# Kernel tuning notes

Measured on AMD Instinct MI355X. Metric: run time of the kernel, lower is better.

Reference implementation:

```python
import jax, jax.numpy as jnp
import numpy as np

NEG_SLOPE = 0.2

def _glorot(key, shape):
    fan_in, fan_out = shape[0], shape[1]
    lim = (6.0 / (fan_in + fan_out)) ** 0.5
    return jax.random.uniform(key, shape, jnp.float32, -lim, lim)

def setup_inputs() -> dict:
    key = jax.random.key(0)
    N, E = 50000, 1000000
    node_dim, edge_dim, hidden = 64, 16, 32
    H1 = 4
    ks = jax.random.split(key, 20)
    x = jax.random.normal(ks[0], (N, node_dim), jnp.float32)
    edge_index = jax.random.randint(ks[1], (2, E), 0, N, jnp.int64)
    edge_attr = jax.random.normal(ks[2], (E, edge_dim), jnp.float32)
    d = dict(x=x, edge_index=edge_index, edge_attr=edge_attr)
    # gat1: GATv2Conv(node_dim -> hidden, heads=4, edge_dim)
    d['W1l'] = _glorot(ks[3], (node_dim, H1 * hidden)); d['b1l'] = jnp.zeros((H1 * hidden,), jnp.float32)
    d['W1r'] = _glorot(ks[4], (node_dim, H1 * hidden)); d['b1r'] = jnp.zeros((H1 * hidden,), jnp.float32)
    d['W1e'] = _glorot(ks[5], (edge_dim, H1 * hidden))
    d['att1'] = _glorot(ks[6], (H1, hidden))
    d['bias1'] = jnp.zeros((H1 * hidden,), jnp.float32)
    # gat2: GATv2Conv(4*hidden -> hidden, heads=1, edge_dim)
    d['W2l'] = _glorot(ks[7], (H1 * hidden, hidden)); d['b2l'] = jnp.zeros((hidden,), jnp.float32)
    d['W2r'] = _glorot(ks[8], (H1 * hidden, hidden)); d['b2r'] = jnp.zeros((hidden,), jnp.float32)
    d['W2e'] = _glorot(ks[9], (edge_dim, hidden))
    d['att2'] = _glorot(ks[10], (1, hidden))
    d['bias2'] = jnp.zeros((hidden,), jnp.float32)
    # edge classifier: Linear(2*hidden+edge_dim -> hidden), ReLU, Linear(hidden -> 1)
    ein = 2 * hidden + edge_dim
    d['Wc1'] = _glorot(ks[11], (ein, hidden)); d['bc1'] = jnp.zeros((hidden,), jnp.float32)
    d['Wc2'] = _glorot(ks[12], (hidden, 1)); d['bc2'] = jnp.zeros((1,), jnp.float32)
    return d

def _gatv2(x, src, dst, eattr, Wl, bl, Wr, br, We, att, bias, H, C):
    # src/dst already include self loops; eattr matches.
    N = x.shape[0]
    xl = (x @ Wl + bl).reshape(N, H, C)   # source transform
    xr = (x @ Wr + br).reshape(N, H, C)   # target transform
    ea = (eattr @ We).reshape(-1, H, C)
    m = jax.nn.leaky_relu(xl[src] + xr[dst] + ea, NEG_SLOPE)   # [E,H,C]
    alpha = jnp.einsum('ehc,hc->eh', m, att)                   # [E,H]
    amax = jax.ops.segment_max(alpha, dst, num_segments=N)
    ealpha = jnp.exp(alpha - amax[dst])
    denom = jax.ops.segment_sum(ealpha, dst, num_segments=N)
    alpha = ealpha / denom[dst]
    out = jax.ops.segment_sum(xl[src] * alpha[..., None], dst, num_segments=N)
    return out.reshape(N, H * C) + bias

def reference(x, edge_index, edge_attr, W1l, b1l, W1r, b1r, W1e, att1, bias1,
              W2l, b2l, W2r, b2r, W2e, att2, bias2, Wc1, bc1, Wc2, bc2):
    N = x.shape[0]
    src, dst = edge_index[0], edge_index[1]
    # add self loops with edge_attr fill_value='mean' (per-target mean of incoming edge attrs)
    loop_attr = jax.ops.segment_sum(edge_attr, dst, num_segments=N)
    deg = jax.ops.segment_sum(jnp.ones((dst.shape[0],), edge_attr.dtype), dst, num_segments=N)
    loop_attr = loop_attr / jnp.maximum(deg, 1.0)[:, None]
    ar = jnp.arange(N, dtype=src.dtype)
    src2 = jnp.concatenate([src, ar]); dst2 = jnp.concatenate([dst, ar])
    eattr2 = jnp.concatenate([edge_attr, loop_attr], axis=0)
    h = _gatv2(x, src2, dst2, eattr2, W1l, b1l, W1r, b1r, W1e, att1, bias1, 4, 32)
    h = jax.nn.elu(h)
    h = _gatv2(h, src2, dst2, eattr2, W2l, b2l, W2r, b2r, W2e, att2, bias2, 1, 32)
    h = jax.nn.elu(h)
    edge_emb = jnp.concatenate([h[src], h[dst]], axis=1)         # [E, 2*hidden]
    feats = jnp.concatenate([edge_emb, edge_attr], axis=1)       # [E, 2*hidden+edge_dim]
    hid = jax.nn.relu(feats @ Wc1 + bc1)
    logits = (hid @ Wc2 + bc2).squeeze(-1)                        # [E]
    return logits
```

## Files before the change

kernel.cpp:

```cpp
#include <hip/hip_runtime.h>

namespace {

constexpr int NN  = 50000;
constexpr int EE  = 1000000;
constexpr int EE2 = EE + NN;
constexpr int ND  = 64;
constexpr int F1  = 128;
constexpr int F2  = 32;
constexpr float NEG = 0.2f;

typedef unsigned short ushort_t;
typedef _Float16 half_t;
typedef _Float16 half2_t __attribute__((ext_vector_type(2)));

__device__ __forceinline__ unsigned short f2h(float f) {
  union { half_t h; unsigned short u; } c; c.h = (half_t)f; return c.u;
}
__device__ __forceinline__ float h2f(unsigned short v) {
  union { unsigned short u; half_t h; } c; c.u = v; return (float)c.h;
}
__device__ __forceinline__ half2_t u2h2(unsigned u) {
  union { unsigned u; half2_t h; } c; c.u = u; return c.h;
}
__device__ __forceinline__ unsigned pack2(float x, float y) {
  return (unsigned)f2h(x) | ((unsigned)f2h(y) << 16);
}
__device__ __forceinline__ half2_t mkh2(float x, float y) {
  half2_t r; r.x = (half_t)x; r.y = (half_t)y; return r;
}

#if __has_builtin(__builtin_amdgcn_fdot2)
#define FDOT2(a, b, c) __builtin_amdgcn_fdot2((a), (b), (c), false)
#else
#define FDOT2(a, b, c) ((float)(a).x * (float)(b).x + (float)(a).y * (float)(b).y + (c))
#endif

__global__ __launch_bounds__(256) void k_deg(const int* __restrict__ ei,
                                             int* __restrict__ deg) {
  int e = blockIdx.x * 256 + threadIdx.x;
  if (e < EE) atomicAdd(&deg[ei[EE + e]], 1);
}

__global__ __launch_bounds__(1024) void k_scan(const int* __restrict__ deg,
                                               int* __restrict__ rowstart) {
  __shared__ int sh[1024];
  int t = threadIdx.x;
  int base = t * 49;
  int end = base + 49; if (end > NN) end = NN;
  int s = 0;
  for (int i = base; i < end; ++i) s += deg[i] + 1;
  sh[t] = s;
  __syncthreads();
  for (int off = 1; off < 1024; off <<= 1) {
    int v = (t >= off) ? sh[t - off] : 0;
    __syncthreads();
    sh[t] += v;
    __syncthreads();
  }
  int run = (t == 0) ? 0 : sh[t - 1];
  for (int i = base; i < end; ++i) { rowstart[i] = run; run += deg[i] + 1; }
  if (t == 1023) rowstart[NN] = sh[1023];
}

__global__ __launch_bounds__(256) void k_fill(const int* __restrict__ ei,
                                              const float* __restrict__ edge_attr,
                                              const int* __restrict__ rowstart,
                                              int* __restrict__ cursor,
                                              int2* __restrict__ esd,
                                              ushort_t* __restrict__ eperm,
                                              int* __restrict__ loopos) {
  int i = blockIdx.x * 256 + threadIdx.x;
  if (i >= EE2) return;
  int sn, d;
  if (i < EE) { sn = ei[i]; d = ei[EE + i]; }
  else        { sn = i - EE; d = sn; }
  int pos = rowstart[d] + atomicAdd(&cursor[d], 1);
  esd[pos] = make_int2(sn, d);
  if (i < EE) {
    const float4* s4 = (const float4*)(edge_attr + (size_t)i * 16);
    float4 a = s4[0], b = s4[1], c = s4[2], e = s4[3];
    uint4 lo, hi;
    lo.x = pack2(a.x, a.y); lo.y = pack2(a.z, a.w);
    lo.z = pack2(b.x, b.y); lo.w = pack2(b.z, b.w);
    hi.x = pack2(c.x, c.y); hi.y = pack2(c.z, c.w);
    hi.z = pack2(e.x, e.y); hi.w = pack2(e.z, e.w);
    uint4* t4 = (uint4*)(eperm + (size_t)pos * 16);
    t4[0] = lo; t4[1] = hi;
  } else {
    loopos[d] = pos;
  }
}

__global__ __launch_bounds__(256) void k_loopattr(const int* __restrict__ rowstart,
                                                  const int* __restrict__ loopos,
                                                  ushort_t* __restrict__ eperm) {
  int tid = blockIdx.x * 256 + threadIdx.x;
  if (tid >= NN * 16) return;
  int n = tid >> 4, k = tid & 15;
  int s = rowstart[n], t = rowstart[n + 1];
  int lp = loopos[n];
  float acc = 0.f;
  for (int i = s; i < t; ++i) {
    if (i != lp) acc += h2f(eperm[(size_t)i * 16 + k]);
  }
  float dg = (float)(t - s - 1);
  eperm[(size_t)lp * 16 + k] = f2h(acc / fmaxf(dg, 1.f));
}

__global__ __launch_bounds__(256) void k_xprep(const float* __restrict__ x,
                                               unsigned* __restrict__ xh) {
  int tid = blockIdx.x * 256 + threadIdx.x;
  if (tid >= NN * 32) return;
  float2 v = ((const float2*)x)[tid];
  xh[tid] = pack2(v.x, v.y);
}

__global__ __launch_bounds__(256) void k_wprep(const float* __restrict__ W1l,
                                               const float* __restrict__ W1r,
                                               const float* __restrict__ W2l,
                                               const float* __restrict__ W2r,
                                               unsigned* __restrict__ W1lp,
                                               unsigned* __restrict__ W1rp,
                                               unsigned* __restrict__ W2lp,
                                               unsigned* __restrict__ W2rp) {
  int tid = blockIdx.x * 256 + threadIdx.x;
  if (tid < 32 * 128) {
    int kp = tid >> 7, j = tid & 127;
    W1lp[tid] = pack2(W1l[(2 * kp) * F1 + j], W1l[(2 * kp + 1) * F1 + j]);
    W1rp[tid] = pack2(W1r[(2 * kp) * F1 + j], W1r[(2 * kp + 1) * F1 + j]);
  }
  if (tid < 64 * 32) {
    int kp = tid >> 5, c = tid & 31;
    W2lp[tid] = pack2(W2l[(2 * kp) * F2 + c], W2l[(2 * kp + 1) * F2 + c]);
    W2rp[tid] = pack2(W2r[(2 * kp) * F2 + c], W2r[(2 * kp + 1) * F2 + c]);
  }
}

__global__ __launch_bounds__(256) void k_xform1(const unsigned* __restrict__ xh,
                                                const unsigned* __restrict__ W1lp,
                                                const unsigned* __restrict__ W1rp,
                                                const float* __restrict__ b1l,
                                                const float* __restrict__ b1r,
                                                ushort_t* __restrict__ xlh,
                                                ushort_t* __restrict__ xrh) {
  int tid = blockIdx.x * 256 + threadIdx.x;
  if (tid >= NN * 32) return;
  int n = tid >> 5, g = tid & 31;
  float4 bl = *(const float4*)(b1l + 4 * g);
  float4 br = *(const float4*)(b1r + 4 * g);
  float al0 = bl.x, al1 = bl.y, al2 = bl.z, al3 = bl.w;
  float ar0 = br.x, ar1 = br.y, ar2 = br.z, ar3 = br.w;
  const uint4* xp = (const uint4*)(xh + (size_t)n * 32);
  const uint4* wl = (const uint4*)W1lp;
  const uint4* wr = (const uint4*)W1rp;
#pragma unroll
  for (int kq = 0; kq < 8; ++kq) {
    uint4 xq = xp[kq];
    unsigned xs[4] = {xq.x, xq.y, xq.z, xq.w};
#pragma unroll
    for (int i = 0; i < 4; ++i) {
      int kp = 4 * kq + i;
      uint4 a = wl[kp * 32 + g];
      uint4 b = wr[kp * 32 + g];
      half2_t xv = u2h2(xs[i]);
      al0 = FDOT2(xv, u2h2(a.x), al0);
      al1 = FDOT2(xv, u2h2(a.y), al1);
      al2 = FDOT2(xv, u2h2(a.z), al2);
      al3 = FDOT2(xv, u2h2(a.w), al3);
      ar0 = FDOT2(xv, u2h2(b.x), ar0);
      ar1 = FDOT2(xv, u2h2(b.y), ar1);
      ar2 = FDOT2(xv, u2h2(b.z), ar2);
      ar3 = FDOT2(xv, u2h2(b.w), ar3);
    }
  }
  uint2 ol, orr;
  ol.x = pack2(al0, al1); ol.y = pack2(al2, al3);
  orr.x = pack2(ar0, ar1); orr.y = pack2(ar2, ar3);
  *(uint2*)(xlh + (size_t)n * F1 + 4 * g) = ol;
  *(uint2*)(xrh + (size_t)n * F1 + 4 * g) = orr;
}

__global__ __launch_bounds__(256, 4) void k_gat1(const ushort_t* __restrict__ eperm,
                                                 const int2* __restrict__ esd,
                                                 const ushort_t* __restrict__ xlh,
                                                 const ushort_t* __restrict__ xrh,
                                                 const float* __restrict__ W1e,
                                                 const float* __restrict__ att1,
                                                 float* __restrict__ h1num,
                                                 float* __restrict__ h1den) {
  int lane = threadIdx.x & 63;
  int h = lane >> 4, q = lane & 15, j = h * 32 + 2 * q;
  half2_t w0p[8], w1p[8];
#pragma unroll
  for (int k = 0; k < 8; ++k) {
    w0p[k] = mkh2(W1e[(2 * k) * F1 + j],     W1e[(2 * k + 1) * F1 + j]);
    w1p[k] = mkh2(W1e[(2 * k) * F1 + j + 1], W1e[(2 * k + 1) * F1 + j + 1]);
  }
  float a0 = att1[j], a1 = att1[j + 1];
  int nw  = (gridDim.x * 256) >> 6;
  int wid = __builtin_amdgcn_readfirstlane((blockIdx.x * 256 + threadIdx.x) >> 6);
  int C = (EE2 + nw - 1) / nw;
  int start = wid * C;
  if (start >= EE2) return;
  int end = min(start + C, EE2);
  const int last = EE2 - 1;

  int2 sdc = esd[start];
  int2 sd1 = esd[min(start + 1, last)];
  const uint4* ep0 = (const uint4*)(eperm + (size_t)start * 16);
  uint4 ca = ep0[0], cb = ep0[1];
  unsigned ul = *(const unsigned*)(xlh + (size_t)sdc.x * F1 + j);
  unsigned ur = *(const unsigned*)(xrh + (size_t)sdc.y * F1 + j);

  int cur = sdc.y;
  float num0 = 0.f, num1 = 0.f, den = 0.f;

  for (int pos = start; pos < end; ++pos) {
    int2 sd2 = esd[min(pos + 2, last)];
    const uint4* epn = (const uint4*)(eperm + (size_t)min(pos + 1, last) * 16);
    uint4 na = epn[0], nb = epn[1];
    unsigned uln = *(const unsigned*)(xlh + (size_t)sd1.x * F1 + j);
    unsigned urn = (sd1.y != sdc.y) ? *(const unsigned*)(xrh + (size_t)sd1.y * F1 + j)
                                    : ur;
    half2_t e2[8];
    e2[0] = u2h2(ca.x); e2[1] = u2h2(ca.y); e2[2] = u2h2(ca.z); e2[3] = u2h2(ca.w);
    e2[4] = u2h2(cb.x); e2[5] = u2h2(cb.y); e2[6] = u2h2(cb.z); e2[7] = u2h2(cb.w);
    float ea0 = 0.f, ea1 = 0.f;
#pragma unroll
    for (int k = 0; k < 8; ++k) {
      ea0 = FDOT2(e2[k], w0p[k], ea0);
      ea1 = FDOT2(e2[k], w1p[k], ea1);
    }
    half2_t ul2 = u2h2(ul), ur2 = u2h2(ur);
    float m0 = (float)ul2.x + (float)ur2.x + ea0;
    float m1 = (float)ul2.y + (float)ur2.y + ea1;
    m0 = fmaxf(m0, NEG * m0);
    m1 = fmaxf(m1, NEG * m1);
    float p = a0 * m0 + a1 * m1;
#pragma unroll
    for (int m = 8; m >= 1; m >>= 1) p += __shfl_xor(p, m);
    float pe = __expf(p);
    if (sdc.y != cur) {
      atomicAdd(&h1num[(size_t)cur * F1 + j], num0);
      atomicAdd(&h1num[(size_t)cur * F1 + j + 1], num1);
      if (q == 0) atomicAdd(&h1den[cur * 4 + h], den);
      num0 = 0.f; num1 = 0.f; den = 0.f;
      cur = sdc.y;
    }
    num0 += pe * (float)ul2.x;
    num1 += pe * (float)ul2.y;
    den  += pe;
    sdc = sd1; sd1 = sd2; ca = na; cb = nb; ul = uln; ur = urn;
  }
  atomicAdd(&h1num[(size_t)cur * F1 + j], num0);
  atomicAdd(&h1num[(size_t)cur * F1 + j + 1], num1);
  if (q == 0) atomicAdd(&h1den[cur * 4 + h], den);
}

__global__ __launch_bounds__(256) void k_gatfin1(const float* __restrict__ h1num,
                                                 const float* __restrict__ h1den,
                                                 const float* __restrict__ bias1,
                                                 unsigned* __restrict__ h1h) {
  int tid = blockIdx.x * 256 + threadIdx.x;
  if (tid >= NN * 64) return;
  int n = tid >> 6, lane = tid & 63;
  float2 nm = *(const float2*)(h1num + (size_t)n * F1 + 2 * lane);
  float den = h1den[n * 4 + (lane >> 4)];
  float2 bs = *(const float2*)(bias1 + 2 * lane);
  float o0 = nm.x / den + bs.x;
  float o1 = nm.y / den + bs.y;
  o0 = o0 > 0.f ? o0 : (__expf(o0) - 1.f);
  o1 = o1 > 0.f ? o1 : (__expf(o1) - 1.f);
  h1h[tid] = pack2(o0, o1);
}

__global__ __launch_bounds__(256) void k_xform2(const unsigned* __restrict__ h1h,
                                                const unsigned* __restrict__ W2lp,
                                                const unsigned* __restrict__ W2rp,
                                                const float* __restrict__ b2l,
                                                const float* __restrict__ b2r,
                                                ushort_t* __restrict__ xl2h,
                                                ushort_t* __restrict__ xr2h) {
  int tid = blockIdx.x * 256 + threadIdx.x;
  if (tid >= NN * 8) return;
  int n = tid >> 3, g = tid & 7;
  float4 bl = *(const float4*)(b2l + 4 * g);
  float4 br = *(const float4*)(b2r + 4 * g);
  float al0 = bl.x, al1 = bl.y, al2 = bl.z, al3 = bl.w;
  float ar0 = br.x, ar1 = br.y, ar2 = br.z, ar3 = br.w;
  const uint4* hp = (const uint4*)(h1h + (size_t)n * 64);
  const uint4* wl = (const uint4*)W2lp;
  const uint4* wr = (const uint4*)W2rp;
#pragma unroll 4
  for (int kq = 0; kq < 16; ++kq) {
    uint4 hq = hp[kq];
    unsigned hs[4] = {hq.x, hq.y, hq.z, hq.w};
#pragma unroll
    for (int i = 0; i < 4; ++i) {
      int kp = 4 * kq + i;
      uint4 a = wl[kp * 8 + g];
      uint4 b = wr[kp * 8 + g];
      half2_t hv = u2h2(hs[i]);
      al0 = FDOT2(hv, u2h2(a.x), al0);
      al1 = FDOT2(hv, u2h2(a.y), al1);
      al2 = FDOT2(hv, u2h2(a.z), al2);
      al3 = FDOT2(hv, u2h2(a.w), al3);
      ar0 = FDOT2(hv, u2h2(b.x), ar0);
      ar1 = FDOT2(hv, u2h2(b.y), ar1);
      ar2 = FDOT2(hv, u2h2(b.z), ar2);
      ar3 = FDOT2(hv, u2h2(b.w), ar3);
    }
  }
  uint2 ol, orr;
  ol.x = pack2(al0, al1); ol.y = pack2(al2, al3);
  orr.x = pack2(ar0, ar1); orr.y = pack2(ar2, ar3);
  *(uint2*)(xl2h + (size_t)n * F2 + 4 * g) = ol;
  *(uint2*)(xr2h + (size_t)n * F2 + 4 * g) = orr;
}

__global__ __launch_bounds__(256, 4) void k_gat2(const ushort_t* __restrict__ eperm,
                                                 const int2* __restrict__ esd,
                                                 const ushort_t* __restrict__ xl2h,
                                                 const ushort_t* __restrict__ xr2h,
                                                 const float* __restrict__ W2e,
                                                 const float* __restrict__ att2,
                                                 float* __restrict__ h2num,
                                                 float* __restrict__ h2den) {
  int lane = threadIdx.x & 63;
  int g = lane >> 4, q = lane & 15, j = 2 * q;
  half2_t w0p[8], w1p[8];
#pragma unroll
  for (int k = 0; k < 8; ++k) {
    w0p[k] = mkh2(W2e[(2 * k) * F2 + j],     W2e[(2 * k + 1) * F2 + j]);
    w1p[k] = mkh2(W2e[(2 * k) * F2 + j + 1], W2e[(2 * k + 1) * F2 + j + 1]);
  }
  float a0 = att2[j], a1 = att2[j + 1];
  int nw  = (gridDim.x * 256) >> 6;
  int wid = (blockIdx.x * 256 + threadIdx.x) >> 6;
  int ngroups = nw * 4;
  int gid = wid * 4 + g;
  int C = (EE2 + ngroups - 1) / ngroups;
  int start = gid * C;
  if (start >= EE2) return;
  int end = min(start + C, EE2);
  const int last = EE2 - 1;

  int2 sdc = esd[start];
  int2 sd1 = esd[min(start + 1, last)];
  const uint4* ep0 = (const uint4*)(eperm + (size_t)start * 16);
  uint4 ca = ep0[0], cb = ep0[1];
  unsigned ul = *(const unsigned*)(xl2h + (size_t)sdc.x * F2 + j);
  unsigned ur = *(const unsigned*)(xr2h + (size_t)sdc.y * F2 + j);

  int cur = sdc.y;
  float num0 = 0.f, num1 = 0.f, den = 0.f;

  for (int pos = start; pos < end; ++pos) {
    int2 sd2 = esd[min(pos + 2, last)];
    const uint4* epn = (const uint4*)(eperm + (size_t)min(pos + 1, last) * 16);
    uint4 na = epn[0], nb = epn[1];
    unsigned uln = *(const unsigned*)(xl2h + (size_t)sd1.x * F2 + j);
    unsigned urn = (sd1.y != sdc.y) ? *(const unsigned*)(xr2h + (size_t)sd1.y * F2 + j)
                                    : ur;
    half2_t e2[8];
    e2[0] = u2h2(ca.x); e2[1] = u2h2(ca.y); e2[2] = u2h2(ca.z); e2[3] = u2h2(ca.w);
    e2[4] = u2h2(cb.x); e2[5] = u2h2(cb.y); e2[6] = u2h2(cb.z); e2[7] = u2h2(cb.w);
    float ea = 0.f, eb = 0.f;
#pragma unroll
    for (int k = 0; k < 8; ++k) {
      ea = FDOT2(e2[k], w0p[k], ea);
      eb = FDOT2(e2[k], w1p[k], eb);
    }
    half2_t ul2 = u2h2(ul), ur2 = u2h2(ur);
    float m0 = (float)ul2.x + (float)ur2.x + ea;
    float m1 = (float)ul2.y + (float)ur2.y + eb;
    m0 = fmaxf(m0, NEG * m0);
    m1 = fmaxf(m1, NEG * m1);
    float p = a0 * m0 + a1 * m1;
#pragma unroll
    for (int m = 8; m >= 1; m >>= 1) p += __shfl_xor(p, m);
    float pe = __expf(p);
    if (sdc.y != cur) {
      atomicAdd(&h2num[(size_t)cur * F2 + j], num0);
      atomicAdd(&h2num[(size_t)cur * F2 + j + 1], num1);
      if (q == 0) atomicAdd(&h2den[cur], den);
      num0 = 0.f; num1 = 0.f; den = 0.f;
      cur = sdc.y;
    }
    num0 += pe * (float)ul2.x;
    num1 += pe * (float)ul2.y;
    den  += pe;
    sdc = sd1; sd1 = sd2; ca = na; cb = nb; ul = uln; ur = urn;
  }
  atomicAdd(&h2num[(size_t)cur * F2 + j], num0);
  atomicAdd(&h2num[(size_t)cur * F2 + j + 1], num1);
  if (q == 0) atomicAdd(&h2den[cur], den);
}

__global__ __launch_bounds__(256) void k_gatfin2(const float* __restrict__ h2num,
                                                 const float* __restrict__ h2den,
                                                 const float* __restrict__ bias2,
                                                 float* __restrict__ h2) {
  int tid = blockIdx.x * 256 + threadIdx.x;
  if (tid >= NN * 16) return;
  int n = tid >> 4, q = tid & 15;
  float2 nm = *(const float2*)(h2num + (size_t)n * F2 + 2 * q);
  float den = h2den[n];
  float2 bs = *(const float2*)(bias2 + 2 * q);
  float o0 = nm.x / den + bs.x;
  float o1 = nm.y / den + bs.y;
  o0 = o0 > 0.f ? o0 : (__expf(o0) - 1.f);
  o1 = o1 > 0.f ? o1 : (__expf(o1) - 1.f);
  *(float2*)(h2 + (size_t)n * F2 + 2 * q) = make_float2(o0, o1);
}

__global__ __launch_bounds__(256) void k_ucls(const float* __restrict__ h2,
                                              const float* __restrict__ Wc1,
                                              float* __restrict__ us,
                                              float* __restrict__ ud) {
  int tid = blockIdx.x * 256 + threadIdx.x;
  if (tid >= NN * F2) return;
  int n = tid >> 5, c = tid & 31;
  const float* hp = h2 + (size_t)n * F2;
  float a = 0.f, b = 0.f;
#pragma unroll 8
  for (int k = 0; k < 32; ++k) {
    float hv = hp[k];
    a += hv * Wc1[k * F2 + c];
    b += hv * Wc1[(32 + k) * F2 + c];
  }
  us[tid] = a;
  ud[tid] = b;
}

__global__ __launch_bounds__(256, 4) void k_cls(const int* __restrict__ ei,
                                                const float* __restrict__ edge_attr,
                                                const float* __restrict__ us,
                                                const float* __restrict__ ud,
                                                const float* __restrict__ Wc1,
                                                const float* __restrict__ bc1,
                                                const float* __restrict__ Wc2,
                                                const float* __restrict__ bc2,
                                                float* __restrict__ out) {
  int lane = threadIdx.x & 63;
  int g = lane >> 4, q = lane & 15, j = 2 * q;
  float wk0[16], wk1[16];
#pragma unroll
  for (int k = 0; k < 16; ++k) {
    wk0[k] = Wc1[(64 + k) * F2 + j];
    wk1[k] = Wc1[(64 + k) * F2 + j + 1];
  }
  float b0 = bc1[j], b1 = bc1[j + 1], c0 = Wc2[j], c1 = Wc2[j + 1];
  float bb = bc2[0];
  int nw  = (gridDim.x * 256) >> 6;
  int wid = __builtin_amdgcn_readfirstlane((blockIdx.x * 256 + threadIdx.x) >> 6);
  int C = (((EE + nw - 1) / nw) + 3) & ~3;
  int start = wid * C;
  if (start >= EE) return;
  int end = min(start + C, EE);
  const int last = EE - 1;

  int e0c = min(start + g, last);
  int sn0 = ei[e0c], dn0 = ei[EE + e0c];
  int e1c = min(start + 4 + g, last);
  int sn1 = ei[e1c], dn1 = ei[EE + e1c];
  const float4* ep0 = (const float4*)(edge_attr + (size_t)e0c * 16);
  float4 ca0 = ep0[0], ca1 = ep0[1], ca2 = ep0[2], ca3 = ep0[3];
  float2 su = *(const float2*)(us + (size_t)sn0 * F2 + j);
  float2 du = *(const float2*)(ud + (size_t)dn0 * F2 + j);

  for (int base = start; base < end; base += 4) {
    int e2c = min(base + 8 + g, last);
    int sn2 = ei[e2c], dn2 = ei[EE + e2c];
    const float4* epn = (const float4*)(edge_attr + (size_t)min(base + 4 + g, last) * 16);
    float4 na0 = epn[0], na1 = epn[1], na2 = epn[2], na3 = epn[3];
    float2 sun = *(const float2*)(us + (size_t)sn1 * F2 + j);
    float2 dun = *(const float2*)(ud + (size_t)dn1 * F2 + j);
    float ev[16] = {ca0.x, ca0.y, ca0.z, ca0.w, ca1.x, ca1.y, ca1.z, ca1.w,
                    ca2.x, ca2.y, ca2.z, ca2.w, ca3.x, ca3.y, ca3.z, ca3.w};
    float acc0 = b0 + su.x + du.x;
    float acc1 = b1 + su.y + du.y;
#pragma unroll
    for (int k = 0; k < 16; ++k) { acc0 += ev[k] * wk0[k]; acc1 += ev[k] * wk1[k]; }
    float r = fmaxf(acc0, 0.f) * c0 + fmaxf(acc1, 0.f) * c1;
#pragma unroll
    for (int m = 8; m >= 1; m >>= 1) r += __shfl_xor(r, m);
    int e = base + g;
    if (q == 0 && e < end) out[e] = r + bb;
    sn1 = sn2; dn1 = dn2;
    ca0 = na0; ca1 = na1; ca2 = na2; ca3 = na3;
    su = sun; du = dun;
  }
}

}

extern "C" void kernel_launch(void* const* d_in, const int* in_sizes, int n_in,
                              void* d_out, int out_size, void* d_ws, size_t ws_size,
                              hipStream_t stream) {
  const float* x         = (const float*)d_in[0];
  const int*   ei        = (const int*)d_in[1];
  const float* edge_attr = (const float*)d_in[2];
  const float* W1l  = (const float*)d_in[3];
  const float* b1l  = (const float*)d_in[4];
  const float* W1r  = (const float*)d_in[5];
  const float* b1r  = (const float*)d_in[6];
  const float* W1e  = (const float*)d_in[7];
  const float* att1 = (const float*)d_in[8];
  const float* bias1= (const float*)d_in[9];
  const float* W2l  = (const float*)d_in[10];
  const float* b2l  = (const float*)d_in[11];
  const float* W2r  = (const float*)d_in[12];
  const float* b2r  = (const float*)d_in[13];
  const float* W2e  = (const float*)d_in[14];
  const float* att2 = (const float*)d_in[15];
  const float* bias2= (const float*)d_in[16];
  const float* Wc1  = (const float*)d_in[17];
  const float* bc1  = (const float*)d_in[18];
  const float* Wc2  = (const float*)d_in[19];
  const float* bc2  = (const float*)d_in[20];
  float* out = (float*)d_out;

  int*  deg      = (int*)d_ws;
  int*  cursor   = deg + NN;
  int*  loopos   = cursor + NN;
  int*  rowstart = loopos + NN;
  int2* esd      = (int2*)(rowstart + 50008);
  ushort_t* eperm = (ushort_t*)(esd + EE2);
  ushort_t* xlh  = eperm + (size_t)EE2 * 16;
  ushort_t* xrh  = xlh + (size_t)NN * F1;
  float* h1num   = (float*)(xrh + (size_t)NN * F1);
  float* h1den   = h1num + (size_t)NN * F1;
  unsigned* h1h  = (unsigned*)(h1den + (size_t)NN * 4);
  unsigned* W1lp = h1h + (size_t)NN * 64;
  unsigned* W1rp = W1lp + 4096;
  unsigned* W2lp = W1rp + 4096;
  unsigned* W2rp = W2lp + 2048;
  unsigned* xh   = (unsigned*)h1num;
  ushort_t* xl2h = xlh;
  ushort_t* xr2h = xl2h + (size_t)NN * F2;
  float* h2num   = h1num;
  float* h2den   = h1num + (size_t)NN * F2;
  float* h2      = h2den + NN;
  float* us      = h2 + (size_t)NN * F2;
  float* ud      = us + (size_t)NN * F2;

  hipMemsetAsync(deg, 0, 2 * (size_t)NN * sizeof(int), stream);

  k_deg<<<(EE + 255) / 256, 256, 0, stream>>>(ei, deg);
  k_scan<<<1, 1024, 0, stream>>>(deg, rowstart);
  k_fill<<<(EE2 + 255) / 256, 256, 0, stream>>>(ei, edge_attr, rowstart, cursor,
                                                esd, eperm, loopos);
  k_loopattr<<<(NN * 16 + 255) / 256, 256, 0, stream>>>(rowstart, loopos, eperm);
  k_xprep<<<(NN * 32 + 255) / 256, 256, 0, stream>>>(x, xh);
  k_wprep<<<16, 256, 0, stream>>>(W1l, W1r, W2l, W2r, W1lp, W1rp, W2lp, W2rp);
  k_xform1<<<(NN * 32 + 255) / 256, 256, 0, stream>>>(xh, W1lp, W1rp, b1l, b1r, xlh, xrh);
  hipMemsetAsync(h1num, 0, (size_t)NN * 132 * sizeof(float), stream);
  k_gat1<<<2048, 256, 0, stream>>>(eperm, esd, xlh, xrh, W1e, att1, h1num, h1den);
  k_gatfin1<<<(NN * 64 + 255) / 256, 256, 0, stream>>>(h1num, h1den, bias1, h1h);
  k_xform2<<<(NN * 8 + 255) / 256, 256, 0, stream>>>(h1h, W2lp, W2rp, b2l, b2r, xl2h, xr2h);
  hipMemsetAsync(h2num, 0, (size_t)NN * 33 * sizeof(float), stream);
  k_gat2<<<2048, 256, 0, stream>>>(eperm, esd, xl2h, xr2h, W2e, att2, h2num, h2den);
  k_gatfin2<<<(NN * 16 + 255) / 256, 256, 0, stream>>>(h2num, h2den, bias2, h2);
  k_ucls<<<(NN * F2 + 255) / 256, 256, 0, stream>>>(h2, Wc1, us, ud);
  k_cls<<<2048, 256, 0, stream>>>(ei, edge_attr, us, ud, Wc1, bc1, Wc2, bc2, out);
}
```

Before: 567.6 us.

## Run classifier over dst-sorted fp16 edge buffer and fuse ELU with classifier projection

The edge classifier now walks the CSR-permuted edge list, reading the fp16 edge attributes already built for the GAT layers instead of the fp32 originals. It reuses the destination projection when consecutive edges share a target, uses packed fp16 dot products, and scatters each result through a new stored original-edge index. The separate gatfin2 and ucls kernels are merged into one kernel that shuffles the ELU outputs to compute the us/ud projections. This cuts edge-attribute traffic and one launch, but adds an index buffer written in fill, a scattered output store, and fp16 rounding in the classifier.

```diff
diff --git a/kernel.cpp b/kernel.cpp
--- a/kernel.cpp
+++ b/kernel.cpp
@@ -68,6 +68,7 @@
                                               const int* __restrict__ rowstart,
                                               int* __restrict__ cursor,
                                               int2* __restrict__ esd,
+                                              int* __restrict__ ebuf,
                                               ushort_t* __restrict__ eperm,
                                               int* __restrict__ loopos) {
   int i = blockIdx.x * 256 + threadIdx.x;
@@ -77,6 +78,7 @@
   else        { sn = i - EE; d = sn; }
   int pos = rowstart[d] + atomicAdd(&cursor[d], 1);
   esd[pos] = make_int2(sn, d);
+  ebuf[pos] = i;
   if (i < EE) {
     const float4* s4 = (const float4*)(edge_attr + (size_t)i * 16);
     float4 a = s4[0], b = s4[1], c = s4[2], e = s4[3];
@@ -398,13 +400,16 @@
   if (q == 0) atomicAdd(&h2den[cur], den);
 }
 
-__global__ __launch_bounds__(256) void k_gatfin2(const float* __restrict__ h2num,
-                                                 const float* __restrict__ h2den,
-                                                 const float* __restrict__ bias2,
-                                                 float* __restrict__ h2) {
+__global__ __launch_bounds__(256) void k_fin2(const float* __restrict__ h2num,
+                                              const float* __restrict__ h2den,
+                                              const float* __restrict__ bias2,
+                                              const float* __restrict__ Wc1,
+                                              float* __restrict__ us,
+                                              float* __restrict__ ud) {
   int tid = blockIdx.x * 256 + threadIdx.x;
   if (tid >= NN * 16) return;
-  int n = tid >> 4, q = tid & 15;
+  int n = tid >> 4, q = threadIdx.x & 15;
+  int lanebase = threadIdx.x & ~15;
   float2 nm = *(const float2*)(h2num + (size_t)n * F2 + 2 * q);
   float den = h2den[n];
   float2 bs = *(const float2*)(bias2 + 2 * q);
@@ -412,30 +417,25 @@
   float o1 = nm.y / den + bs.y;
   o0 = o0 > 0.f ? o0 : (__expf(o0) - 1.f);
   o1 = o1 > 0.f ? o1 : (__expf(o1) - 1.f);
-  *(float2*)(h2 + (size_t)n * F2 + 2 * q) = make_float2(o0, o1);
-}
-
-__global__ __launch_bounds__(256) void k_ucls(const float* __restrict__ h2,
-                                              const float* __restrict__ Wc1,
-                                              float* __restrict__ us,
-                                              float* __restrict__ ud) {
-  int tid = blockIdx.x * 256 + threadIdx.x;
-  if (tid >= NN * F2) return;
-  int n = tid >> 5, c = tid & 31;
-  const float* hp = h2 + (size_t)n * F2;
-  float a = 0.f, b = 0.f;
-#pragma unroll 8
-  for (int k = 0; k < 32; ++k) {
-    float hv = hp[k];
-    a += hv * Wc1[k * F2 + c];
-    b += hv * Wc1[(32 + k) * F2 + c];
-  }
-  us[tid] = a;
-  ud[tid] = b;
-}
-
-__global__ __launch_bounds__(256, 4) void k_cls(const int* __restrict__ ei,
-                                                const float* __restrict__ edge_attr,
+  int c0i = 2 * q, c1i = 2 * q + 1;
+  float us0 = 0.f, us1 = 0.f, ud0 = 0.f, ud1 = 0.f;
+#pragma unroll
+  for (int kq = 0; kq < 16; ++kq) {
+    float h0 = __shfl(o0, lanebase + kq);
+    float h1 = __shfl(o1, lanebase + kq);
+    int k0 = 2 * kq, k1 = 2 * kq + 1;
+    us0 += h0 * Wc1[k0 * F2 + c0i] + h1 * Wc1[k1 * F2 + c0i];
+    us1 += h0 * Wc1[k0 * F2 + c1i] + h1 * Wc1[k1 * F2 + c1i];
+    ud0 += h0 * Wc1[(32 + k0) * F2 + c0i] + h1 * Wc1[(32 + k1) * F2 + c0i];
+    ud1 += h0 * Wc1[(32 + k0) * F2 + c1i] + h1 * Wc1[(32 + k1) * F2 + c1i];
+  }
+  *(float2*)(us + (size_t)n * F2 + 2 * q) = make_float2(us0, us1);
+  *(float2*)(ud + (size_t)n * F2 + 2 * q) = make_float2(ud0, ud1);
+}
+
+__global__ __launch_bounds__(256, 4) void k_cls(const ushort_t* __restrict__ eperm,
+                                                const int2* __restrict__ esd,
+                                                const int* __restrict__ ebuf,
                                                 const float* __restrict__ us,
                                                 const float* __restrict__ ud,
                                                 const float* __restrict__ Wc1,
@@ -445,52 +445,57 @@
                                                 float* __restrict__ out) {
   int lane = threadIdx.x & 63;
   int g = lane >> 4, q = lane & 15, j = 2 * q;
-  float wk0[16], wk1[16];
-#pragma unroll
-  for (int k = 0; k < 16; ++k) {
-    wk0[k] = Wc1[(64 + k) * F2 + j];
-    wk1[k] = Wc1[(64 + k) * F2 + j + 1];
+  half2_t wkp0[8], wkp1[8];
+#pragma unroll
+  for (int k = 0; k < 8; ++k) {
+    wkp0[k] = mkh2(Wc1[(64 + 2 * k) * F2 + j],     Wc1[(64 + 2 * k + 1) * F2 + j]);
+    wkp1[k] = mkh2(Wc1[(64 + 2 * k) * F2 + j + 1], Wc1[(64 + 2 * k + 1) * F2 + j + 1]);
   }
   float b0 = bc1[j], b1 = bc1[j + 1], c0 = Wc2[j], c1 = Wc2[j + 1];
   float bb = bc2[0];
   int nw  = (gridDim.x * 256) >> 6;
-  int wid = __builtin_amdgcn_readfirstlane((blockIdx.x * 256 + threadIdx.x) >> 6);
-  int C = (((EE + nw - 1) / nw) + 3) & ~3;
-  int start = wid * C;
-  if (start >= EE) return;
-  int end = min(start + C, EE);
-  const int last = EE - 1;
-
-  int e0c = min(start + g, last);
-  int sn0 = ei[e0c], dn0 = ei[EE + e0c];
-  int e1c = min(start + 4 + g, last);
-  int sn1 = ei[e1c], dn1 = ei[EE + e1c];
-  const float4* ep0 = (const float4*)(edge_attr + (size_t)e0c * 16);
-  float4 ca0 = ep0[0], ca1 = ep0[1], ca2 = ep0[2], ca3 = ep0[3];
-  float2 su = *(const float2*)(us + (size_t)sn0 * F2 + j);
-  float2 du = *(const float2*)(ud + (size_t)dn0 * F2 + j);
-
-  for (int base = start; base < end; base += 4) {
-    int e2c = min(base + 8 + g, last);
-    int sn2 = ei[e2c], dn2 = ei[EE + e2c];
-    const float4* epn = (const float4*)(edge_attr + (size_t)min(base + 4 + g, last) * 16);
-    float4 na0 = epn[0], na1 = epn[1], na2 = epn[2], na3 = epn[3];
-    float2 sun = *(const float2*)(us + (size_t)sn1 * F2 + j);
-    float2 dun = *(const float2*)(ud + (size_t)dn1 * F2 + j);
-    float ev[16] = {ca0.x, ca0.y, ca0.z, ca0.w, ca1.x, ca1.y, ca1.z, ca1.w,
-                    ca2.x, ca2.y, ca2.z, ca2.w, ca3.x, ca3.y, ca3.z, ca3.w};
+  int wid = (blockIdx.x * 256 + threadIdx.x) >> 6;
+  int ngroups = nw * 4;
+  int gid = wid * 4 + g;
+  int C = (EE2 + ngroups - 1) / ngroups;
+  int start = gid * C;
+  if (start >= EE2) return;
+  int end = min(start + C, EE2);
+  const int last = EE2 - 1;
+
+  int2 sdc = esd[start];
+  int2 sd1 = esd[min(start + 1, last)];
+  int ec = ebuf[start];
+  int e1 = ebuf[min(start + 1, last)];
+  const uint4* ep0 = (const uint4*)(eperm + (size_t)start * 16);
+  uint4 ca = ep0[0], cb = ep0[1];
+  float2 su = *(const float2*)(us + (size_t)sdc.x * F2 + j);
+  float2 du = *(const float2*)(ud + (size_t)sdc.y * F2 + j);
+
+  for (int pos = start; pos < end; ++pos) {
+    int2 sd2 = esd[min(pos + 2, last)];
+    int e2i = ebuf[min(pos + 2, last)];
+    const uint4* epn = (const uint4*)(eperm + (size_t)min(pos + 1, last) * 16);
+    uint4 na = epn[0], nb = epn[1];
+    float2 sun = *(const float2*)(us + (size_t)sd1.x * F2 + j);
+    float2 dun = (sd1.y != sdc.y) ? *(const float2*)(ud + (size_t)sd1.y * F2 + j)
+                                  : du;
+    half2_t e2[8];
+    e2[0] = u2h2(ca.x); e2[1] = u2h2(ca.y); e2[2] = u2h2(ca.z); e2[3] = u2h2(ca.w);
+    e2[4] = u2h2(cb.x); e2[5] = u2h2(cb.y); e2[6] = u2h2(cb.z); e2[7] = u2h2(cb.w);
     float acc0 = b0 + su.x + du.x;
     float acc1 = b1 + su.y + du.y;
 #pragma unroll
-    for (int k = 0; k < 16; ++k) { acc0 += ev[k] * wk0[k]; acc1 += ev[k] * wk1[k]; }
+    for (int k = 0; k < 8; ++k) {
+      acc0 = FDOT2(e2[k], wkp0[k], acc0);
+      acc1 = FDOT2(e2[k], wkp1[k], acc1);
+    }
     float r = fmaxf(acc0, 0.f) * c0 + fmaxf(acc1, 0.f) * c1;
 #pragma unroll
     for (int m = 8; m >= 1; m >>= 1) r += __shfl_xor(r, m);
-    int e = base + g;
-    if (q == 0 && e < end) out[e] = r + bb;
-    sn1 = sn2; dn1 = dn2;
-    ca0 = na0; ca1 = na1; ca2 = na2; ca3 = na3;
-    su = sun; du = dun;
+    if (q == 0 && ec < EE) out[ec] = r + bb;
+    sdc = sd1; sd1 = sd2; ec = e1; e1 = e2i;
+    ca = na; cb = nb; su = sun; du = dun;
   }
 }
 
@@ -527,7 +532,8 @@
   int*  loopos   = cursor + NN;
   int*  rowstart = loopos + NN;
   int2* esd      = (int2*)(rowstart + 50008);
-  ushort_t* eperm = (ushort_t*)(esd + EE2);
+  int*  ebuf     = (int*)(esd + EE2);
+  ushort_t* eperm = (ushort_t*)(ebuf + EE2 + 4);
   ushort_t* xlh  = eperm + (size_t)EE2 * 16;
   ushort_t* xrh  = xlh + (size_t)NN * F1;
   float* h1num   = (float*)(xrh + (size_t)NN * F1);
@@ -542,8 +548,7 @@
   ushort_t* xr2h = xl2h + (size_t)NN * F2;
   float* h2num   = h1num;
   float* h2den   = h1num + (size_t)NN * F2;
-  float* h2      = h2den + NN;
-  float* us      = h2 + (size_t)NN * F2;
+  float* us      = h2den + NN;
   float* ud      = us + (size_t)NN * F2;
 
   hipMemsetAsync(deg, 0, 2 * (size_t)NN * sizeof(int), stream);
@@ -551,7 +556,7 @@
   k_deg<<<(EE + 255) / 256, 256, 0, stream>>>(ei, deg);
   k_scan<<<1, 1024, 0, stream>>>(deg, rowstart);
   k_fill<<<(EE2 + 255) / 256, 256, 0, stream>>>(ei, edge_attr, rowstart, cursor,
-                                                esd, eperm, loopos);
+                                                esd, ebuf, eperm, loopos);
   k_loopattr<<<(NN * 16 + 255) / 256, 256, 0, stream>>>(rowstart, loopos, eperm);
   k_xprep<<<(NN * 32 + 255) / 256, 256, 0, stream>>>(x, xh);
   k_wprep<<<16, 256, 0, stream>>>(W1l, W1r, W2l, W2r, W1lp, W1rp, W2lp, W2rp);
@@ -562,7 +567,6 @@
   k_xform2<<<(NN * 8 + 255) / 256, 256, 0, stream>>>(h1h, W2lp, W2rp, b2l, b2r, xl2h, xr2h);
   hipMemsetAsync(h2num, 0, (size_t)NN * 33 * sizeof(float), stream);
   k_gat2<<<2048, 256, 0, stream>>>(eperm, esd, xl2h, xr2h, W2e, att2, h2num, h2den);
-  k_gatfin2<<<(NN * 16 + 255) / 256, 256, 0, stream>>>(h2num, h2den, bias2, h2);
-  k_ucls<<<(NN * F2 + 255) / 256, 256, 0, stream>>>(h2, Wc1, us, ud);
-  k_cls<<<2048, 256, 0, stream>>>(ei, edge_attr, us, ud, Wc1, bc1, Wc2, bc2, out);
-}
+  k_fin2<<<(NN * 16 + 255) / 256, 256, 0, stream>>>(h2num, h2den, bias2, Wc1, us, ud);
+  k_cls<<<2048, 256, 0, stream>>>(eperm, esd, ebuf, us, ud, Wc1, bc1, Wc2, bc2, out);
+}
```

Result: slower. 579.5 us (+2.1%).

## Partition GAT edge loops on node boundaries and fuse softmax finalize into aggregation

Applied to the files above, without the earlier changes.

The GAT aggregation kernels now use binary search over rowstart so each worker owns whole destination nodes. The normalization, bias and ELU are then computed inline and written directly, with no atomics into num/den buffers. This removes two memsets, two finalize kernels and all float atomics, and shrinks the workspace. Chunk sizes now vary with node boundaries, so load balance can be uneven on high-degree nodes. The us/ud projection kernel is also rewritten to use shuffles with two outputs per thread.

```diff
diff --git a/kernel.cpp b/kernel.cpp
--- a/kernel.cpp
+++ b/kernel.cpp
@@ -35,6 +35,15 @@
 #else
 #define FDOT2(a, b, c) ((float)(a).x * (float)(b).x + (float)(a).y * (float)(b).y + (c))
 #endif
+
+__device__ __forceinline__ int lbound(const int* __restrict__ rowstart, int target) {
+  int lo = 0, hi = NN;
+  while (lo < hi) {
+    int mid = (lo + hi) >> 1;
+    if (rowstart[mid] < target) lo = mid + 1; else hi = mid;
+  }
+  return lo;
+}
 
 __global__ __launch_bounds__(256) void k_deg(const int* __restrict__ ei,
                                              int* __restrict__ deg) {
@@ -185,10 +194,11 @@
                                                  const int2* __restrict__ esd,
                                                  const ushort_t* __restrict__ xlh,
                                                  const ushort_t* __restrict__ xrh,
+                                                 const int* __restrict__ rowstart,
                                                  const float* __restrict__ W1e,
                                                  const float* __restrict__ att1,
-                                                 float* __restrict__ h1num,
-                                                 float* __restrict__ h1den) {
+                                                 const float* __restrict__ bias1,
+                                                 unsigned* __restrict__ h1h) {
   int lane = threadIdx.x & 63;
   int h = lane >> 4, q = lane & 15, j = h * 32 + 2 * q;
   half2_t w0p[8], w1p[8];
@@ -198,25 +208,30 @@
     w1p[k] = mkh2(W1e[(2 * k) * F1 + j + 1], W1e[(2 * k + 1) * F1 + j + 1]);
   }
   float a0 = att1[j], a1 = att1[j + 1];
+  float2 bs = *(const float2*)(bias1 + 2 * lane);
   int nw  = (gridDim.x * 256) >> 6;
   int wid = __builtin_amdgcn_readfirstlane((blockIdx.x * 256 + threadIdx.x) >> 6);
   int C = (EE2 + nw - 1) / nw;
-  int start = wid * C;
-  if (start >= EE2) return;
-  int end = min(start + C, EE2);
+  int tA = wid * C;
+  if (tA >= EE2) return;
+  int tB = min(tA + C, EE2);
+  int nA = lbound(rowstart, tA);
+  int nB = lbound(rowstart, tB);
+  if (nA >= nB) return;
+  int s0 = rowstart[nA], s1 = rowstart[nB];
   const int last = EE2 - 1;
 
-  int2 sdc = esd[start];
-  int2 sd1 = esd[min(start + 1, last)];
-  const uint4* ep0 = (const uint4*)(eperm + (size_t)start * 16);
+  int n = nA;
+  int nend = rowstart[nA + 1];
+  int2 sdc = esd[s0];
+  int2 sd1 = esd[min(s0 + 1, last)];
+  const uint4* ep0 = (const uint4*)(eperm + (size_t)s0 * 16);
   uint4 ca = ep0[0], cb = ep0[1];
   unsigned ul = *(const unsigned*)(xlh + (size_t)sdc.x * F1 + j);
   unsigned ur = *(const unsigned*)(xrh + (size_t)sdc.y * F1 + j);
-
-  int cur = sdc.y;
   float num0 = 0.f, num1 = 0.f, den = 0.f;
 
-  for (int pos = start; pos < end; ++pos) {
+  for (int pos = s0; pos < s1; ++pos) {
     int2 sd2 = esd[min(pos + 2, last)];
     const uint4* epn = (const uint4*)(eperm + (size_t)min(pos + 1, last) * 16);
     uint4 na = epn[0], nb = epn[1];
@@ -241,38 +256,21 @@
 #pragma unroll
     for (int m = 8; m >= 1; m >>= 1) p += __shfl_xor(p, m);
     float pe = __expf(p);
-    if (sdc.y != cur) {
-      atomicAdd(&h1num[(size_t)cur * F1 + j], num0);
-      atomicAdd(&h1num[(size_t)cur * F1 + j + 1], num1);
-      if (q == 0) atomicAdd(&h1den[cur * 4 + h], den);
-      num0 = 0.f; num1 = 0.f; den = 0.f;
-      cur = sdc.y;
-    }
     num0 += pe * (float)ul2.x;
     num1 += pe * (float)ul2.y;
     den  += pe;
+    if (pos + 1 == nend) {
+      float o0 = num0 / den + bs.x;
+      float o1 = num1 / den + bs.y;
+      o0 = o0 > 0.f ? o0 : (__expf(o0) - 1.f);
+      o1 = o1 > 0.f ? o1 : (__expf(o1) - 1.f);
+      h1h[(size_t)n * 64 + lane] = pack2(o0, o1);
+      ++n;
+      nend = rowstart[n + 1];
+      num0 = 0.f; num1 = 0.f; den = 0.f;
+    }
     sdc = sd1; sd1 = sd2; ca = na; cb = nb; ul = uln; ur = urn;
   }
-  atomicAdd(&h1num[(size_t)cur * F1 + j], num0);
-  atomicAdd(&h1num[(size_t)cur * F1 + j + 1], num1);
-  if (q == 0) atomicAdd(&h1den[cur * 4 + h], den);
-}
-
-__global__ __launch_bounds__(256) void k_gatfin1(const float* __restrict__ h1num,
-                                                 const float* __restrict__ h1den,
-                                                 const float* __restrict__ bias1,
-                                                 unsigned* __restrict__ h1h) {
-  int tid = blockIdx.x * 256 + threadIdx.x;
-  if (tid >= NN * 64) return;
-  int n = tid >> 6, lane = tid & 63;
-  float2 nm = *(const float2*)(h1num + (size_t)n * F1 + 2 * lane);
-  float den = h1den[n * 4 + (lane >> 4)];
-  float2 bs = *(const float2*)(bias1 + 2 * lane);
-  float o0 = nm.x / den + bs.x;
-  float o1 = nm.y / den + bs.y;
-  o0 = o0 > 0.f ? o0 : (__expf(o0) - 1.f);
-  o1 = o1 > 0.f ? o1 : (__expf(o1) - 1.f);
-  h1h[tid] = pack2(o0, o1);
 }
 
 __global__ __launch_bounds__(256) void k_xform2(const unsigned* __restrict__ h1h,
@@ -323,10 +321,11 @@
                                                  const int2* __restrict__ esd,
                                                  const ushort_t* __restrict__ xl2h,
                                                  const ushort_t* __restrict__ xr2h,
+                                                 const int* __restrict__ rowstart,
                                                  const float* __restrict__ W2e,
                                                  const float* __restrict__ att2,
-                                                 float* __restrict__ h2num,
-                                                 float* __restrict__ h2den) {
+                                                 const float* __restrict__ bias2,
+                                                 float* __restrict__ h2) {
   int lane = threadIdx.x & 63;
   int g = lane >> 4, q = lane & 15, j = 2 * q;
   half2_t w0p[8], w1p[8];
@@ -336,27 +335,32 @@
     w1p[k] = mkh2(W2e[(2 * k) * F2 + j + 1], W2e[(2 * k + 1) * F2 + j + 1]);
   }
   float a0 = att2[j], a1 = att2[j + 1];
+  float2 bs = *(const float2*)(bias2 + 2 * q);
   int nw  = (gridDim.x * 256) >> 6;
   int wid = (blockIdx.x * 256 + threadIdx.x) >> 6;
   int ngroups = nw * 4;
   int gid = wid * 4 + g;
   int C = (EE2 + ngroups - 1) / ngroups;
-  int start = gid * C;
-  if (start >= EE2) return;
-  int end = min(start + C, EE2);
+  int tA = gid * C;
+  if (tA >= EE2) return;
+  int tB = min(tA + C, EE2);
+  int nA = lbound(rowstart, tA);
+  int nB = lbound(rowstart, tB);
+  if (nA >= nB) return;
+  int s0 = rowstart[nA], s1 = rowstart[nB];
   const int last = EE2 - 1;
 
-  int2 sdc = esd[start];
-  int2 sd1 = esd[min(start + 1, last)];
-  const uint4* ep0 = (const uint4*)(eperm + (size_t)start * 16);
+  int n = nA;
+  int nend = rowstart[nA + 1];
+  int2 sdc = esd[s0];
+  int2 sd1 = esd[min(s0 + 1, last)];
+  const uint4* ep0 = (const uint4*)(eperm + (size_t)s0 * 16);
   uint4 ca = ep0[0], cb = ep0[1];
   unsigned ul = *(const unsigned*)(xl2h + (size_t)sdc.x * F2 + j);
   unsigned ur = *(const unsigned*)(xr2h + (size_t)sdc.y * F2 + j);
-
-  int cur = sdc.y;
   float num0 = 0.f, num1 = 0.f, den = 0.f;
 
-  for (int pos = start; pos < end; ++pos) {
+  for (int pos = s0; pos < s1; ++pos) {
     int2 sd2 = esd[min(pos + 2, last)];
     const uint4* epn = (const uint4*)(eperm + (size_t)min(pos + 1, last) * 16);
     uint4 na = epn[0], nb = epn[1];
@@ -381,57 +385,46 @@
 #pragma unroll
     for (int m = 8; m >= 1; m >>= 1) p += __shfl_xor(p, m);
     float pe = __expf(p);
-    if (sdc.y != cur) {
-      atomicAdd(&h2num[(size_t)cur * F2 + j], num0);
-      atomicAdd(&h2num[(size_t)cur * F2 + j + 1], num1);
-      if (q == 0) atomicAdd(&h2den[cur], den);
-      num0 = 0.f; num1 = 0.f; den = 0.f;
-      cur = sdc.y;
-    }
     num0 += pe * (float)ul2.x;
     num1 += pe * (float)ul2.y;
     den  += pe;
+    if (pos + 1 == nend) {
+      float o0 = num0 / den + bs.x;
+      float o1 = num1 / den + bs.y;
+      o0 = o0 > 0.f ? o0 : (__expf(o0) - 1.f);
+      o1 = o1 > 0.f ? o1 : (__expf(o1) - 1.f);
+      *(float2*)(h2 + (size_t)n * F2 + 2 * q) = make_float2(o0, o1);
+      ++n;
+      nend = rowstart[n + 1];
+      num0 = 0.f; num1 = 0.f; den = 0.f;
+    }
     sdc = sd1; sd1 = sd2; ca = na; cb = nb; ul = uln; ur = urn;
   }
-  atomicAdd(&h2num[(size_t)cur * F2 + j], num0);
-  atomicAdd(&h2num[(size_t)cur * F2 + j + 1], num1);
-  if (q == 0) atomicAdd(&h2den[cur], den);
-}
-
-__global__ __launch_bounds__(256) void k_gatfin2(const float* __restrict__ h2num,
-                                                 const float* __restrict__ h2den,
-                                                 const float* __restrict__ bias2,
-                                                 float* __restrict__ h2) {
-  int tid = blockIdx.x * 256 + threadIdx.x;
-  if (tid >= NN * 16) return;
-  int n = tid >> 4, q = tid & 15;
-  float2 nm = *(const float2*)(h2num + (size_t)n * F2 + 2 * q);
-  float den = h2den[n];
-  float2 bs = *(const float2*)(bias2 + 2 * q);
-  float o0 = nm.x / den + bs.x;
-  float o1 = nm.y / den + bs.y;
-  o0 = o0 > 0.f ? o0 : (__expf(o0) - 1.f);
-  o1 = o1 > 0.f ? o1 : (__expf(o1) - 1.f);
-  *(float2*)(h2 + (size_t)n * F2 + 2 * q) = make_float2(o0, o1);
-}
-
-__global__ __launch_bounds__(256) void k_ucls(const float* __restrict__ h2,
+}
+
+__global__ __launch_bounds__(256) void k_fin2(const float* __restrict__ h2,
                                               const float* __restrict__ Wc1,
                                               float* __restrict__ us,
                                               float* __restrict__ ud) {
   int tid = blockIdx.x * 256 + threadIdx.x;
-  if (tid >= NN * F2) return;
-  int n = tid >> 5, c = tid & 31;
-  const float* hp = h2 + (size_t)n * F2;
-  float a = 0.f, b = 0.f;
-#pragma unroll 8
-  for (int k = 0; k < 32; ++k) {
-    float hv = hp[k];
-    a += hv * Wc1[k * F2 + c];
-    b += hv * Wc1[(32 + k) * F2 + c];
-  }
-  us[tid] = a;
-  ud[tid] = b;
+  if (tid >= NN * 16) return;
+  int n = tid >> 4, q = threadIdx.x & 15;
+  int lanebase = threadIdx.x & ~15;
+  float2 hv = *(const float2*)(h2 + (size_t)n * F2 + 2 * q);
+  int c0i = 2 * q, c1i = 2 * q + 1;
+  float us0 = 0.f, us1 = 0.f, ud0 = 0.f, ud1 = 0.f;
+#pragma unroll
+  for (int kq = 0; kq < 16; ++kq) {
+    float h0 = __shfl(hv.x, lanebase + kq);
+    float h1 = __shfl(hv.y, lanebase + kq);
+    int k0 = 2 * kq, k1 = 2 * kq + 1;
+    us0 += h0 * Wc1[k0 * F2 + c0i] + h1 * Wc1[k1 * F2 + c0i];
+    us1 += h0 * Wc1[k0 * F2 + c1i] + h1 * Wc1[k1 * F2 + c1i];
+    ud0 += h0 * Wc1[(32 + k0) * F2 + c0i] + h1 * Wc1[(32 + k1) * F2 + c0i];
+    ud1 += h0 * Wc1[(32 + k0) * F2 + c1i] + h1 * Wc1[(32 + k1) * F2 + c1i];
+  }
+  *(float2*)(us + (size_t)n * F2 + 2 * q) = make_float2(us0, us1);
+  *(float2*)(ud + (size_t)n * F2 + 2 * q) = make_float2(ud0, ud1);
 }
 
 __global__ __launch_bounds__(256, 4) void k_cls(const int* __restrict__ ei,
@@ -530,21 +523,17 @@
   ushort_t* eperm = (ushort_t*)(esd + EE2);
   ushort_t* xlh  = eperm + (size_t)EE2 * 16;
   ushort_t* xrh  = xlh + (size_t)NN * F1;
-  float* h1num   = (float*)(xrh + (size_t)NN * F1);
-  float* h1den   = h1num + (size_t)NN * F1;
-  unsigned* h1h  = (unsigned*)(h1den + (size_t)NN * 4);
-  unsigned* W1lp = h1h + (size_t)NN * 64;
+  unsigned* h1h  = (unsigned*)(xrh + (size_t)NN * F1);
+  unsigned* xh   = h1h + (size_t)NN * 64;
+  unsigned* W1lp = xh + (size_t)NN * 32;
   unsigned* W1rp = W1lp + 4096;
   unsigned* W2lp = W1rp + 4096;
   unsigned* W2rp = W2lp + 2048;
-  unsigned* xh   = (unsigned*)h1num;
+  float* h2      = (float*)(W2rp + 2048);
+  float* us      = h2 + (size_t)NN * F2;
+  float* ud      = us + (size_t)NN * F2;
   ushort_t* xl2h = xlh;
   ushort_t* xr2h = xl2h + (size_t)NN * F2;
-  float* h2num   = h1num;
-  float* h2den   = h1num + (size_t)NN * F2;
-  float* h2      = h2den + NN;
-  float* us      = h2 + (size_t)NN * F2;
-  float* ud      = us + (size_t)NN * F2;
 
   hipMemsetAsync(deg, 0, 2 * (size_t)NN * sizeof(int), stream);
 
@@ -556,13 +545,9 @@
   k_xprep<<<(NN * 32 + 255) / 256, 256, 0, stream>>>(x, xh);
   k_wprep<<<16, 256, 0, stream>>>(W1l, W1r, W2l, W2r, W1lp, W1rp, W2lp, W2rp);
   k_xform1<<<(NN * 32 + 255) / 256, 256, 0, stream>>>(xh, W1lp, W1rp, b1l, b1r, xlh, xrh);
-  hipMemsetAsync(h1num, 0, (size_t)NN * 132 * sizeof(float), stream);
-  k_gat1<<<2048, 256, 0, stream>>>(eperm, esd, xlh, xrh, W1e, att1, h1num, h1den);
-  k_gatfin1<<<(NN * 64 + 255) / 256, 256, 0, stream>>>(h1num, h1den, bias1, h1h);
+  k_gat1<<<2048, 256, 0, stream>>>(eperm, esd, xlh, xrh, rowstart, W1e, att1, bias1, h1h);
   k_xform2<<<(NN * 8 + 255) / 256, 256, 0, stream>>>(h1h, W2lp, W2rp, b2l, b2r, xl2h, xr2h);
-  hipMemsetAsync(h2num, 0, (size_t)NN * 33 * sizeof(float), stream);
-  k_gat2<<<2048, 256, 0, stream>>>(eperm, esd, xl2h, xr2h, W2e, att2, h2num, h2den);
-  k_gatfin2<<<(NN * 16 + 255) / 256, 256, 0, stream>>>(h2num, h2den, bias2, h2);
-  k_ucls<<<(NN * F2 + 255) / 256, 256, 0, stream>>>(h2, Wc1, us, ud);
+  k_gat2<<<2048, 256, 0, stream>>>(eperm, esd, xl2h, xr2h, rowstart, W2e, att2, bias2, h2);
+  k_fin2<<<(NN * 16 + 255) / 256, 256, 0, stream>>>(h2, Wc1, us, ud);
   k_cls<<<2048, 256, 0, stream>>>(ei, edge_attr, us, ud, Wc1, bc1, Wc2, bc2, out);
 }
```

Result: slower. 595.6 us (+4.9%).
